# Performance work log

Hardware: AMD Instinct MI355X
Metric: run time of the kernel (lower is better)

## Reference

```python
import jax, jax.numpy as jnp
import numpy as np

B, T, U, D = 8, 200, 50, 512
INNER, VOCAB = 640, 1024


def setup_inputs() -> dict:
    key = jax.random.key(0)
    k1, k2, k3, k4 = jax.random.split(key, 4)
    enc_outputs = jax.random.normal(k1, (B, T, D), dtype=jnp.float32)
    dec_outputs = jax.random.normal(k2, (B, U, D), dtype=jnp.float32)
    # Dense(inner_dim, activation='tanh') params
    W1 = jax.random.normal(k3, (D, INNER), dtype=jnp.float32) / np.sqrt(D)
    b1 = jnp.zeros((INNER,), dtype=jnp.float32)
    # Dense(vocab_size) params
    W2 = jax.random.normal(k4, (INNER, VOCAB), dtype=jnp.float32) / np.sqrt(INNER)
    b2 = jnp.zeros((VOCAB,), dtype=jnp.float32)
    return {"enc_outputs": enc_outputs, "dec_outputs": dec_outputs,
            "W1": W1, "b1": b1, "W2": W2, "b2": b2}


def reference(enc_outputs, dec_outputs, W1, b1, W2, b2):
    # joint_inputs: (B, T, U, D) via broadcast add, exactly as the TF module
    joint = enc_outputs[:, :, None, :] + dec_outputs[:, None, :, :]
    hidden = jnp.tanh(jnp.einsum('btud,dh->btuh', joint, W1) + b1)  # (B,T,U,INNER)
    logits = jnp.einsum('btuh,hv->btuv', hidden, W2) + b2            # (B,T,U,VOCAB)
    return logits
```

## Files before the change

kernel.cpp:

```cpp
#include <hip/hip_runtime.h>
#include <hip/hip_bf16.h>
#include <stdint.h>

namespace {

constexpr int B = 8, T = 200, U = 50, D = 512, INNER = 640, VOCAB = 1024;
constexpr int M_TOTAL = B * T * U;
constexpr int ROWS_E = B * T;
constexpr int ROWS_D = B * U;
constexpr int ROWS_ED = ROWS_E + ROWS_D;
constexpr int BM = 64, BN = 512;
constexpr int CK = 128;
constexpr int NCHUNK = INNER / CK;
constexpr int CHUNK_B = 16 * 1024;

typedef __bf16 bf16x8 __attribute__((ext_vector_type(8)));
typedef float  f32x4  __attribute__((ext_vector_type(4)));
typedef unsigned short u16;
typedef unsigned int   u32;

__device__ __forceinline__ u16 f2bf(float f) {
  uint32_t u = __float_as_uint(f);
  uint32_t rounding = 0x7FFFu + ((u >> 16) & 1u);
  return (u16)((u + rounding) >> 16);
}

__device__ __forceinline__ float fast_tanh(float x) {
  float e = __expf(2.0f * x);
  float r = __builtin_amdgcn_rcpf(e + 1.0f);
  return 1.0f - 2.0f * r;
}

__global__ __launch_bounds__(320) void k_prep(const float* __restrict__ enc,
                                              const float* __restrict__ dec,
                                              const float* __restrict__ W1,
                                              const float* __restrict__ b1,
                                              const float* __restrict__ W2,
                                              float* __restrict__ ED,
                                              u16* __restrict__ W2B) {
  if (blockIdx.x >= 500) {
    const int idx = (blockIdx.x - 500) * 320 + threadIdx.x;
    const int lane = idx & 63;
    const int f = idx >> 6;
    const int ks = f >> 6;
    const int nf = f & 63;
    const int n = nf * 16 + (lane & 15);
    const int k = ks * 32 + (lane >> 4) * 8;
    u16 v[8];
#pragma unroll
    for (int j = 0; j < 8; ++j)
      v[j] = f2bf(W2[(size_t)(k + j) * VOCAB + n]);
    uint64_t lo = (uint64_t)v[0] | ((uint64_t)v[1] << 16) |
                  ((uint64_t)v[2] << 32) | ((uint64_t)v[3] << 48);
    uint64_t hi = (uint64_t)v[4] | ((uint64_t)v[5] << 16) |
                  ((uint64_t)v[6] << 32) | ((uint64_t)v[7] << 48);
    uint64_t* dst = reinterpret_cast<uint64_t*>(W2B + (size_t)idx * 8);
    dst[0] = lo;
    dst[1] = hi;
    return;
  }

  __shared__ float rows[4 * D];
  const int r0 = blockIdx.x * 4;
  const bool is_enc = (r0 < ROWS_E);
  const float* src = is_enc ? (enc + (size_t)r0 * D)
                            : (dec + (size_t)(r0 - ROWS_E) * D);
  for (int i = threadIdx.x; i < 4 * D; i += 320) rows[i] = src[i];
  __syncthreads();

  const int c0 = threadIdx.x, c1 = threadIdx.x + 320;
  float acc[4][2];
  const float bias0 = is_enc ? b1[c0] : 0.f;
  const float bias1 = is_enc ? b1[c1] : 0.f;
#pragma unroll
  for (int r = 0; r < 4; ++r) { acc[r][0] = bias0; acc[r][1] = bias1; }

  for (int d = 0; d < D; d += 8) {
    f32x4 rv[4][2];
#pragma unroll
    for (int r = 0; r < 4; ++r) {
      rv[r][0] = *reinterpret_cast<const f32x4*>(&rows[r * D + d]);
      rv[r][1] = *reinterpret_cast<const f32x4*>(&rows[r * D + d + 4]);
    }
#pragma unroll
    for (int dd = 0; dd < 8; ++dd) {
      const float w0 = W1[(size_t)(d + dd) * INNER + c0];
      const float w1 = W1[(size_t)(d + dd) * INNER + c1];
#pragma unroll
      for (int r = 0; r < 4; ++r) {
        const float x = rv[r][dd >> 2][dd & 3];
        acc[r][0] = fmaf(x, w0, acc[r][0]);
        acc[r][1] = fmaf(x, w1, acc[r][1]);
      }
    }
  }
#pragma unroll
  for (int r = 0; r < 4; ++r) {
    ED[(size_t)(r0 + r) * INNER + c0] = acc[r][0];
    ED[(size_t)(r0 + r) * INNER + c1] = acc[r][1];
  }
}

__global__ __launch_bounds__(512, 4) void k_main(const float* __restrict__ ED,
                                                 const u16* __restrict__ W2B,
                                                 const float* __restrict__ b2,
                                                 float* __restrict__ out) {
  __shared__ u16 At[2 * CHUNK_B / 2];
  char* At_b = reinterpret_cast<char*>(At);

  const int tid = threadIdx.x;
  const int m0 = blockIdx.x * BM;
  const int n0 = blockIdx.y * BN;

  const int row0 = tid >> 4;
  const int g    = tid & 15;
  int eoff[2], doff[2], wbyte[2];
#pragma unroll
  for (int i = 0; i < 2; ++i) {
    const int row = row0 + i * 32;
    const int m = m0 + row;
    const int b = m / (T * U);
    const int rem = m - b * (T * U);
    const int t = rem / U;
    const int u = rem - t * U;
    eoff[i] = (b * T + t) * INNER;
    doff[i] = (ROWS_E + b * U + u) * INNER;
    wbyte[i] = (((row >> 4) * 4 + (g >> 2)) << 10) + ((g & 3) * 16 + (row & 15)) * 16;
  }

  auto tanh_chunk = [&](int c, int bufsel) __attribute__((always_inline)) {
    const int kb = c * CK + g * 8;
#pragma unroll
    for (int i = 0; i < 2; ++i) {
      const float* E = ED + eoff[i] + kb;
      const float* Dp = ED + doff[i] + kb;
      const f32x4 e0 = *reinterpret_cast<const f32x4*>(E);
      const f32x4 e1 = *reinterpret_cast<const f32x4*>(E + 4);
      const f32x4 d0 = *reinterpret_cast<const f32x4*>(Dp);
      const f32x4 d1 = *reinterpret_cast<const f32x4*>(Dp + 4);
      const u32 p0 = (u32)f2bf(fast_tanh(e0[0] + d0[0])) |
                     ((u32)f2bf(fast_tanh(e0[1] + d0[1])) << 16);
      const u32 p1 = (u32)f2bf(fast_tanh(e0[2] + d0[2])) |
                     ((u32)f2bf(fast_tanh(e0[3] + d0[3])) << 16);
      const u32 p2 = (u32)f2bf(fast_tanh(e1[0] + d1[0])) |
                     ((u32)f2bf(fast_tanh(e1[1] + d1[1])) << 16);
      const u32 p3 = (u32)f2bf(fast_tanh(e1[2] + d1[2])) |
                     ((u32)f2bf(fast_tanh(e1[3] + d1[3])) << 16);
      int4 pk; pk.x = (int)p0; pk.y = (int)p1; pk.z = (int)p2; pk.w = (int)p3;
      *reinterpret_cast<int4*>(At_b + bufsel * CHUNK_B + wbyte[i]) = pk;
    }
  };

  const int lane = tid & 63;
  const int w    = tid >> 6;
  const int llo  = lane & 15;
  const int lhi  = lane >> 4;
  const u16* Bp = W2B + ((size_t)((n0 >> 4) + w * 4) << 9) + lane * 8;

  f32x4 acc[4][4];
#pragma unroll
  for (int mi = 0; mi < 4; ++mi)
#pragma unroll
    for (int ni = 0; ni < 4; ++ni) acc[mi][ni] = (f32x4){0.f, 0.f, 0.f, 0.f};

  tanh_chunk(0, 0);
  __syncthreads();

  for (int c = 0; c < NCHUNK; ++c) {
    const int ab = (c & 1) * CHUNK_B;
    if (c < NCHUNK - 1) tanh_chunk(c + 1, (c + 1) & 1);

#pragma unroll
    for (int ks = 0; ks < 4; ++ks) {
      bf16x8 bfr[4], a[4];
#pragma unroll
      for (int ni = 0; ni < 4; ++ni)
        bfr[ni] = *reinterpret_cast<const bf16x8*>(
            Bp + ((size_t)((c * 4 + ks) * 64 + ni) << 9));
#pragma unroll
      for (int mi = 0; mi < 4; ++mi)
        a[mi] = *reinterpret_cast<const bf16x8*>(
            At_b + ab + ((mi * 4 + ks) << 10) + lane * 16);
#pragma unroll
      for (int mi = 0; mi < 4; ++mi)
#pragma unroll
        for (int ni = 0; ni < 4; ++ni)
          acc[mi][ni] = __builtin_amdgcn_mfma_f32_16x16x32_bf16(a[mi], bfr[ni], acc[mi][ni], 0, 0, 0);
    }
    __syncthreads();
  }

  float b2v[4];
#pragma unroll
  for (int ni = 0; ni < 4; ++ni) b2v[ni] = b2[n0 + w * 64 + ni * 16 + llo];

#pragma unroll
  for (int mi = 0; mi < 4; ++mi) {
#pragma unroll
    for (int q = 0; q < 4; ++q) {
      const int row = m0 + mi * 16 + lhi * 4 + q;
      float* orow = out + (size_t)row * VOCAB + n0 + w * 64 + llo;
#pragma unroll
      for (int ni = 0; ni < 4; ++ni)
        __builtin_nontemporal_store(acc[mi][ni][q] + b2v[ni], orow + ni * 16);
    }
  }
}

}

extern "C" void kernel_launch(void* const* d_in, const int* in_sizes, int n_in,
                              void* d_out, int out_size, void* d_ws, size_t ws_size,
                              hipStream_t stream) {
  const float* enc = (const float*)d_in[0];
  const float* dec = (const float*)d_in[1];
  const float* W1  = (const float*)d_in[2];
  const float* b1  = (const float*)d_in[3];
  const float* W2  = (const float*)d_in[4];
  const float* b2  = (const float*)d_in[5];
  float* out = (float*)d_out;

  float* ED  = (float*)d_ws;
  u16*   W2B = (u16*)((char*)d_ws + (size_t)ROWS_ED * INNER * 4);

  hipLaunchKernelGGL(k_prep, dim3(756), dim3(320), 0, stream,
                     enc, dec, W1, b1, W2, ED, W2B);
  hipLaunchKernelGGL(k_main, dim3(M_TOTAL / BM, VOCAB / BN), dim3(512), 0, stream,
                     ED, W2B, b2, out);
}
```

Baseline: 178.6 us.

## Materialize bf16 tanh hidden in workspace and run LDS-free GEMM with XCD-aware tiling

Splits the fused tanh+GEMM into two kernels. A new kernel writes the bf16 hidden activations, already in MFMA fragment layout, to a workspace buffer. The main GEMM then reads A fragments straight from global memory with register prefetch and no shared memory or barriers. It also uses 128x256 tiles and an XCD-aware block remapping so neighbouring tiles share L2. This avoids recomputing tanh once per N-tile and removes the LDS sync, at the cost of an extra ~82MB round trip through HBM; the old fused path is kept as a fallback when the workspace is too small.

```diff
diff --git a/kernel.cpp b/kernel.cpp
--- a/kernel.cpp
+++ b/kernel.cpp
@@ -9,15 +9,17 @@
 constexpr int ROWS_E = B * T;
 constexpr int ROWS_D = B * U;
 constexpr int ROWS_ED = ROWS_E + ROWS_D;
-constexpr int BM = 64, BN = 512;
-constexpr int CK = 128;
-constexpr int NCHUNK = INNER / CK;
-constexpr int CHUNK_B = 16 * 1024;
 
 typedef __bf16 bf16x8 __attribute__((ext_vector_type(8)));
 typedef float  f32x4  __attribute__((ext_vector_type(4)));
+typedef int    i32x4  __attribute__((ext_vector_type(4)));
 typedef unsigned short u16;
 typedef unsigned int   u32;
+
+constexpr size_t ED_BYTES  = (size_t)ROWS_ED * INNER * 4;
+constexpr size_t W2B_BYTES = (size_t)VOCAB * INNER * 2;
+constexpr size_t H_BYTES   = (size_t)M_TOTAL * INNER * 2;
+constexpr size_t WS_NEED   = ED_BYTES + W2B_BYTES + H_BYTES;
 
 __device__ __forceinline__ u16 f2bf(float f) {
   uint32_t u = __float_as_uint(f);
@@ -101,16 +103,122 @@
   }
 }
 
-__global__ __launch_bounds__(512, 4) void k_main(const float* __restrict__ ED,
+__global__ __launch_bounds__(256) void k_h(const float* __restrict__ ED,
+                                           u16* __restrict__ H) {
+  const int lane = threadIdx.x & 63;
+  const int mg = blockIdx.x * 4 + (threadIdx.x >> 6);
+  const int m = mg * 16 + (lane & 15);
+  const int b = m / (T * U);
+  const int rem = m - b * (T * U);
+  const int t = rem / U;
+  const int u = rem - t * U;
+  const float* E  = ED + (size_t)(b * T + t) * INNER + (lane >> 4) * 8;
+  const float* Dv = ED + (size_t)(ROWS_E + b * U + u) * INNER + (lane >> 4) * 8;
+  u16* W = H + (size_t)mg * 20 * 512 + lane * 8;
+
+#pragma unroll 4
+  for (int ksg = 0; ksg < 20; ++ksg) {
+    const f32x4 e0 = *reinterpret_cast<const f32x4*>(E + ksg * 32);
+    const f32x4 e1 = *reinterpret_cast<const f32x4*>(E + ksg * 32 + 4);
+    const f32x4 d0 = *reinterpret_cast<const f32x4*>(Dv + ksg * 32);
+    const f32x4 d1 = *reinterpret_cast<const f32x4*>(Dv + ksg * 32 + 4);
+    i32x4 pk;
+    pk.x = (int)((u32)f2bf(fast_tanh(e0[0] + d0[0])) |
+                 ((u32)f2bf(fast_tanh(e0[1] + d0[1])) << 16));
+    pk.y = (int)((u32)f2bf(fast_tanh(e0[2] + d0[2])) |
+                 ((u32)f2bf(fast_tanh(e0[3] + d0[3])) << 16));
+    pk.z = (int)((u32)f2bf(fast_tanh(e1[0] + d1[0])) |
+                 ((u32)f2bf(fast_tanh(e1[1] + d1[1])) << 16));
+    pk.w = (int)((u32)f2bf(fast_tanh(e1[2] + d1[2])) |
+                 ((u32)f2bf(fast_tanh(e1[3] + d1[3])) << 16));
+    __builtin_nontemporal_store(pk, reinterpret_cast<i32x4*>(W + (size_t)ksg * 512));
+  }
+}
+
+__global__ __launch_bounds__(512, 4) void k_main(const u16* __restrict__ H,
                                                  const u16* __restrict__ W2B,
                                                  const float* __restrict__ b2,
                                                  float* __restrict__ out) {
+  const int bid = blockIdx.x;
+  const int xcd = bid & 7;
+  const int idx = bid >> 3;
+  const int wg = (xcd < 4) ? xcd * 313 + idx : 4 * 313 + (xcd - 4) * 312 + idx;
+  const int n0 = (wg & 3) * 256;
+  const int mt = wg >> 2;
+
+  const int tid  = threadIdx.x;
+  const int lane = tid & 63;
+  const int wid  = tid >> 6;
+  const int wr = wid >> 2, wc = wid & 3;
+  const int llo = lane & 15, lhi = lane >> 4;
+
+  const u16* Ap = H + ((size_t)(mt * 8 + wr * 4) * 20) * 512 + lane * 8;
+  const u16* Bq = W2B + ((size_t)((n0 >> 4) + wc * 4)) * 512 + lane * 8;
+
+  f32x4 acc[4][4];
+#pragma unroll
+  for (int mi = 0; mi < 4; ++mi)
+#pragma unroll
+    for (int ni = 0; ni < 4; ++ni) acc[mi][ni] = (f32x4){0.f, 0.f, 0.f, 0.f};
+
+  bf16x8 a[4];
+#pragma unroll
+  for (int mi = 0; mi < 4; ++mi)
+    a[mi] = *reinterpret_cast<const bf16x8*>(Ap + (size_t)mi * 10240);
+
+#pragma unroll
+  for (int ks = 0; ks < 20; ++ks) {
+    bf16x8 bfr[4];
+#pragma unroll
+    for (int ni = 0; ni < 4; ++ni)
+      bfr[ni] = *reinterpret_cast<const bf16x8*>(
+          Bq + (size_t)ks * 32768 + ni * 512);
+    bf16x8 an[4];
+    if (ks < 19) {
+#pragma unroll
+      for (int mi = 0; mi < 4; ++mi)
+        an[mi] = *reinterpret_cast<const bf16x8*>(
+            Ap + (size_t)mi * 10240 + (ks + 1) * 512);
+    }
+#pragma unroll
+    for (int mi = 0; mi < 4; ++mi)
+#pragma unroll
+      for (int ni = 0; ni < 4; ++ni)
+        acc[mi][ni] = __builtin_amdgcn_mfma_f32_16x16x32_bf16(a[mi], bfr[ni], acc[mi][ni], 0, 0, 0);
+    if (ks < 19) {
+#pragma unroll
+      for (int mi = 0; mi < 4; ++mi) a[mi] = an[mi];
+    }
+  }
+
+  float b2v[4];
+#pragma unroll
+  for (int ni = 0; ni < 4; ++ni) b2v[ni] = b2[n0 + wc * 64 + ni * 16 + llo];
+
+#pragma unroll
+  for (int mi = 0; mi < 4; ++mi) {
+#pragma unroll
+    for (int q = 0; q < 4; ++q) {
+      const int row = mt * 128 + wr * 64 + mi * 16 + lhi * 4 + q;
+      float* orow = out + (size_t)row * VOCAB + n0 + wc * 64 + llo;
+#pragma unroll
+      for (int ni = 0; ni < 4; ++ni)
+        __builtin_nontemporal_store(acc[mi][ni][q] + b2v[ni], orow + ni * 16);
+    }
+  }
+}
+
+__global__ __launch_bounds__(512, 4) void k_main_fused(const float* __restrict__ ED,
+                                                       const u16* __restrict__ W2B,
+                                                       const float* __restrict__ b2,
+                                                       float* __restrict__ out) {
+  constexpr int CK = 128, NCHUNK = 5, CHUNK_B = 16 * 1024;
   __shared__ u16 At[2 * CHUNK_B / 2];
   char* At_b = reinterpret_cast<char*>(At);
 
   const int tid = threadIdx.x;
-  const int m0 = blockIdx.x * BM;
-  const int n0 = blockIdx.y * BN;
+  const int m0 = blockIdx.x * 64;
+  const int n0 = blockIdx.y * 512;
 
   const int row0 = tid >> 4;
   const int g    = tid & 15;
@@ -169,7 +277,6 @@
   for (int c = 0; c < NCHUNK; ++c) {
     const int ab = (c & 1) * CHUNK_B;
     if (c < NCHUNK - 1) tanh_chunk(c + 1, (c + 1) & 1);
-
 #pragma unroll
     for (int ks = 0; ks < 4; ++ks) {
       bf16x8 bfr[4], a[4];
@@ -193,7 +300,6 @@
   float b2v[4];
 #pragma unroll
   for (int ni = 0; ni < 4; ++ni) b2v[ni] = b2[n0 + w * 64 + ni * 16 + llo];
-
 #pragma unroll
   for (int mi = 0; mi < 4; ++mi) {
 #pragma unroll
@@ -221,10 +327,18 @@
   float* out = (float*)d_out;
 
   float* ED  = (float*)d_ws;
-  u16*   W2B = (u16*)((char*)d_ws + (size_t)ROWS_ED * INNER * 4);
+  u16*   W2B = (u16*)((char*)d_ws + ED_BYTES);
+  u16*   H   = (u16*)((char*)d_ws + ED_BYTES + W2B_BYTES);
 
   hipLaunchKernelGGL(k_prep, dim3(756), dim3(320), 0, stream,
                      enc, dec, W1, b1, W2, ED, W2B);
-  hipLaunchKernelGGL(k_main, dim3(M_TOTAL / BM, VOCAB / BN), dim3(512), 0, stream,
-                     ED, W2B, b2, out);
-}
+
+  if (ws_size >= WS_NEED) {
+    hipLaunchKernelGGL(k_h, dim3(1250), dim3(256), 0, stream, ED, H);
+    hipLaunchKernelGGL(k_main, dim3(2500), dim3(512), 0, stream,
+                       H, W2B, b2, out);
+  } else {
+    hipLaunchKernelGGL(k_main_fused, dim3(M_TOTAL / 64, VOCAB / 512), dim3(512),
+                       0, stream, ED, W2B, b2, out);
+  }
+}
```

Result: slower. 336.1 us (+88.2%).
